# Kernel optimization log

Measured on AMD Instinct MI355X. Metric: run time of the kernel, lower is better.

Reference implementation:

```python
import jax, jax.numpy as jnp
import numpy as np

HEAD_DIM = 16

def setup_inputs() -> dict:
    key = jax.random.key(0)
    ks = jax.random.split(key, 6)
    b, m, n, e, k, d = 2, 2048, 2048, 128, 8, HEAD_DIM
    # xavier-uniform-like scale for [e, d] fan
    s = float(np.sqrt(6.0 / (e + d)))
    return {
        "x": jax.random.normal(ks[0], (b, m, e), dtype=jnp.float32),
        "y": jax.random.normal(ks[1], (b, n, e), dtype=jnp.float32),
        "lambda1": jax.random.uniform(ks[2], (k, e, d), jnp.float32, -s, s),
        "lambda2": jax.random.uniform(ks[3], (k, e, d), jnp.float32, -s, s),
        "theta1": jax.random.uniform(ks[4], (k, e, d), jnp.float32, -s, s),
        "theta2": jax.random.uniform(ks[5], (k, e, d), jnp.float32, -s, s),
        "bias_lambda": jnp.zeros((k, d), jnp.float32),
        "bias_theta": jnp.zeros((k, d), jnp.float32),
    }

def reference(x, y, lambda1, lambda2, theta1, theta2, bias_lambda, bias_theta):
    head_dim = lambda1.shape[-1]
    # r: [b, m, k, d]
    r = jnp.einsum('bmp,kpd->bmkd', x, lambda1) + bias_lambda
    # dot_att: [k, b, m, n] (bilinear QK via per-head projections of x and y)
    dot_att = jnp.einsum('bmkd,kqd,bnq->kbmn', r, lambda2, y)
    dot_att = dot_att * (head_dim ** -0.5)
    # softmax over the query/m axis (-2), NOT the key axis
    att = jax.nn.softmax(dot_att, axis=-2)
    # combine: [b, n, k, d]
    r2 = jnp.einsum('kbmn,bmp,kpd->bnkd', att, x, theta1) + bias_theta
    # output: [b, n, emb_dim_x]
    return jnp.einsum('bnkd,kqd->bnq', r2, theta2)
```

## Files before the change

kernel.cpp:

```cpp
#include <hip/hip_runtime.h>
#include <math.h>

#define BB 2
#define MM 2048
#define NN 2048
#define EE 128
#define KH 8
#define DD 16
#define NHEADS (BB * KH)
#define MSPLIT 8
#define MCHUNK (MM / MSPLIT)
#define LOG2E 1.44269504088896340736f
#define QSCALE (0.25f * LOG2E)
#define DEFER_THR 8.0f

typedef __bf16 bf16x8 __attribute__((ext_vector_type(8)));
typedef __bf16 bf16x4 __attribute__((ext_vector_type(4)));
typedef float  f32x16 __attribute__((ext_vector_type(16)));
typedef float  f32x4  __attribute__((ext_vector_type(4)));

__device__ inline bf16x8 cvt8(float4 a, float4 b) {
    bf16x8 r;
    r[0] = (__bf16)a.x; r[1] = (__bf16)a.y; r[2] = (__bf16)a.z; r[3] = (__bf16)a.w;
    r[4] = (__bf16)b.x; r[5] = (__bf16)b.y; r[6] = (__bf16)b.z; r[7] = (__bf16)b.w;
    return r;
}

__global__ __launch_bounds__(256) void proj_kernel(
    const float* __restrict__ x, const float* __restrict__ y,
    const float* __restrict__ lambda1, const float* __restrict__ lambda2,
    const float* __restrict__ theta1, const float* __restrict__ bias_lambda,
    __bf16* __restrict__ rK, __bf16* __restrict__ kyQ, __bf16* __restrict__ Vt)
{
    const int grp  = blockIdx.x;
    const int f    = blockIdx.y;
    const int head = blockIdx.z;
    const int b = head >> 3, kh = head & 7;
    const int wave = threadIdx.x >> 6;
    const int lane = threadIdx.x & 63;
    const int l15 = lane & 15, g4 = lane >> 4;

    const float* W   = ((f == 0) ? lambda1 : (f == 1) ? theta1 : lambda2)
                       + (size_t)kh * EE * DD;
    const float* src = ((f == 2) ? y : x) + (size_t)b * MM * EE;

    bf16x8 wf[4];
    #pragma unroll
    for (int kb = 0; kb < 4; ++kb) {
        const float* wp = W + (size_t)(32 * kb + 8 * g4) * DD + l15;
        bf16x8 t;
        #pragma unroll
        for (int e = 0; e < 8; ++e) t[e] = (__bf16)wp[e * DD];
        wf[kb] = t;
    }
    const float bl = (f == 0) ? bias_lambda[kh * DD + l15] : 0.f;

    for (int i = 0; i < 4; ++i) {
        const int m0 = (grp * 16 + wave * 4 + i) * 16;
        const float* xp = src + (size_t)(m0 + l15) * EE + 8 * g4;

        f32x4 acc;
        #pragma unroll
        for (int r = 0; r < 4; ++r) acc[r] = 0.f;

        #pragma unroll
        for (int kb = 0; kb < 4; ++kb) {
            float4 a = *(const float4*)(xp + 32 * kb);
            float4 c = *(const float4*)(xp + 32 * kb + 4);
            bf16x8 xf = cvt8(a, c);
            if (f == 1) acc = __builtin_amdgcn_mfma_f32_16x16x32_bf16(wf[kb], xf, acc, 0, 0, 0);
            else        acc = __builtin_amdgcn_mfma_f32_16x16x32_bf16(xf, wf[kb], acc, 0, 0, 0);
        }

        if (f == 0) {
            #pragma unroll
            for (int r = 0; r < 4; ++r)
                rK[((size_t)head * MM + m0 + 4 * g4 + r) * DD + l15] = (__bf16)(acc[r] + bl);
        } else if (f == 2) {
            #pragma unroll
            for (int r = 0; r < 4; ++r)
                kyQ[((size_t)head * NN + m0 + 4 * g4 + r) * DD + l15] = (__bf16)(acc[r] * QSCALE);
        } else {
            #pragma unroll
            for (int r = 0; r < 4; ++r)
                Vt[((size_t)head * DD + 4 * g4 + r) * MM + m0 + l15] = (__bf16)acc[r];
        }
    }
}

__global__ __launch_bounds__(256) void attn_kernel(
    const __bf16* __restrict__ rK, const __bf16* __restrict__ kyQ,
    const __bf16* __restrict__ Vt,
    float* __restrict__ Opart, float* __restrict__ mlP)
{
    __shared__ __bf16 Pst[4][32][40];

    const int tid  = threadIdx.x;
    const int wave = tid >> 6;
    const int lane = tid & 63;
    const int head = blockIdx.x >> 4;
    const int nbase = (blockIdx.x & 15) * 128 + wave * 32;
    const int ms   = blockIdx.y;
    const int b = head >> 3, kh = head & 7;

    const int l31 = lane & 31;
    const int hi  = lane >> 5;
    const int l15 = lane & 15;
    const int g4  = lane >> 4;

    const bf16x8 qf = *reinterpret_cast<const bf16x8*>(
        kyQ + ((size_t)head * NN + nbase + l31) * DD + 8 * hi);

    f32x4 o0, o1;
    #pragma unroll
    for (int i = 0; i < 4; ++i) { o0[i] = 0.f; o1[i] = 0.f; }
    float mmax = -INFINITY, lsum = 0.f;

    const __bf16* kb = rK + (size_t)head * MM * DD;
    const __bf16* vb = Vt + (size_t)head * DD * MM;

    for (int it = 0; it < MCHUNK / 32; ++it) {
        const int m0 = ms * MCHUNK + it * 32;

        const bf16x8 kf = *reinterpret_cast<const bf16x8*>(
            kb + ((size_t)(m0 + l31)) * DD + 8 * hi);

        f32x16 s;
        #pragma unroll
        for (int i = 0; i < 16; ++i) s[i] = 0.f;
        s = __builtin_amdgcn_mfma_f32_32x32x16_bf16(kf, qf, s, 0, 0, 0);

        float tm = s[0];
        #pragma unroll
        for (int r = 1; r < 16; ++r) tm = fmaxf(tm, s[r]);
        tm = fmaxf(tm, __shfl_xor(tm, 32));

        if (!__all(tm - mmax <= DEFER_THR)) {
            const float newm = fmaxf(mmax, tm);
            const float c = exp2f(mmax - newm);
            lsum *= c;
            #pragma unroll
            for (int r = 0; r < 4; ++r) {
                o0[r] *= __shfl(c, 4 * g4 + r);
                o1[r] *= __shfl(c, 16 + 4 * g4 + r);
            }
            mmax = newm;
        }

        float p[16];
        float ps = 0.f;
        #pragma unroll
        for (int r = 0; r < 16; ++r) { p[r] = exp2f(s[r] - mmax); ps += p[r]; }
        ps += __shfl_xor(ps, 32);
        lsum += ps;

        #pragma unroll
        for (int qd = 0; qd < 4; ++qd) {
            bf16x4 pk;
            pk[0] = (__bf16)p[4 * qd + 0];
            pk[1] = (__bf16)p[4 * qd + 1];
            pk[2] = (__bf16)p[4 * qd + 2];
            pk[3] = (__bf16)p[4 * qd + 3];
            *reinterpret_cast<bf16x4*>(&Pst[wave][l31][8 * qd + 4 * hi]) = pk;
        }

        const bf16x8 vf = *reinterpret_cast<const bf16x8*>(
            vb + (size_t)l15 * MM + m0 + 8 * g4);

        const bf16x8 pa0 = *reinterpret_cast<const bf16x8*>(&Pst[wave][l15][8 * g4]);
        const bf16x8 pa1 = *reinterpret_cast<const bf16x8*>(&Pst[wave][16 + l15][8 * g4]);

        o0 = __builtin_amdgcn_mfma_f32_16x16x32_bf16(pa0, vf, o0, 0, 0, 0);
        o1 = __builtin_amdgcn_mfma_f32_16x16x32_bf16(pa1, vf, o1, 0, 0, 0);
    }

    float* obase = Opart + (((size_t)ms * BB + b) * NN) * (KH * DD) + kh * DD;
    #pragma unroll
    for (int r = 0; r < 4; ++r) {
        const int n0 = nbase + 4 * g4 + r;
        const int n1 = n0 + 16;
        obase[(size_t)n0 * (KH * DD) + l15] = o0[r];
        obase[(size_t)n1 * (KH * DD) + l15] = o1[r];
    }
    if (lane < 32) {
        const size_t mlbase = (((size_t)ms * BB + b) * NN + nbase + l31) * (KH * 2) + kh * 2;
        mlP[mlbase]     = mmax;
        mlP[mlbase + 1] = lsum;
    }
}

__global__ __launch_bounds__(256) void combine_kernel(
    const float* __restrict__ Opart, const float* __restrict__ mlP,
    const float* __restrict__ bias_theta, const float* __restrict__ theta2,
    float* __restrict__ out)
{
    __shared__ float r2s[4][128];

    const int blk = blockIdx.x;
    const int b   = blk >> 9;
    const int n0  = (blk & 511) * 4;
    const int tid = threadIdx.x;

    if (tid < 128) {
        const int n_loc = tid >> 5;
        const int k  = (tid >> 2) & 7;
        const int dq = tid & 3;
        const int n = n0 + n_loc;

        float mm[MSPLIT], ls[MSPLIT];
        float Mx = -INFINITY;
        #pragma unroll
        for (int s = 0; s < MSPLIT; ++s) {
            const size_t base = (((size_t)s * BB + b) * NN + n) * (KH * 2) + k * 2;
            mm[s] = mlP[base];
            ls[s] = mlP[base + 1];
            Mx = fmaxf(Mx, mm[s]);
        }
        float L = 0.f;
        float4 O = make_float4(0.f, 0.f, 0.f, 0.f);
        #pragma unroll
        for (int s = 0; s < MSPLIT; ++s) {
            const float w = exp2f(mm[s] - Mx);
            L = fmaf(ls[s], w, L);
            const float4 op = *(const float4*)(
                Opart + (((size_t)s * BB + b) * NN + n) * (KH * DD) + k * DD + dq * 4);
            O.x = fmaf(w, op.x, O.x); O.y = fmaf(w, op.y, O.y);
            O.z = fmaf(w, op.z, O.z); O.w = fmaf(w, op.w, O.w);
        }
        const float inv = 1.f / L;
        const float* bt = bias_theta + k * DD + dq * 4;
        float4 res;
        res.x = fmaf(O.x, inv, bt[0]);
        res.y = fmaf(O.y, inv, bt[1]);
        res.z = fmaf(O.z, inv, bt[2]);
        res.w = fmaf(O.w, inv, bt[3]);
        *(float4*)&r2s[n_loc][k * DD + dq * 4] = res;
    }
    __syncthreads();
    {
        const int q   = tid & 127;
        const int nl0 = tid >> 7;
        float acc0 = 0.f, acc1 = 0.f;
        #pragma unroll
        for (int k = 0; k < KH; ++k) {
            const float4* t2 = (const float4*)(theta2 + ((size_t)k * EE + q) * DD);
            const float4* ra = (const float4*)&r2s[nl0][k * DD];
            const float4* rb = (const float4*)&r2s[nl0 + 2][k * DD];
            #pragma unroll
            for (int j = 0; j < 4; ++j) {
                const float4 t = t2[j];
                const float4 a = ra[j];
                const float4 bq = rb[j];
                acc0 = fmaf(a.x, t.x, acc0);  acc0 = fmaf(a.y, t.y, acc0);
                acc0 = fmaf(a.z, t.z, acc0);  acc0 = fmaf(a.w, t.w, acc0);
                acc1 = fmaf(bq.x, t.x, acc1); acc1 = fmaf(bq.y, t.y, acc1);
                acc1 = fmaf(bq.z, t.z, acc1); acc1 = fmaf(bq.w, t.w, acc1);
            }
        }
        out[((size_t)b * NN + n0 + nl0) * EE + q]     = acc0;
        out[((size_t)b * NN + n0 + nl0 + 2) * EE + q] = acc1;
    }
}

extern "C" void kernel_launch(void* const* d_in, const int* in_sizes, int n_in,
                              void* d_out, int out_size, void* d_ws, size_t ws_size,
                              hipStream_t stream) {
    const float* x           = (const float*)d_in[0];
    const float* y           = (const float*)d_in[1];
    const float* lambda1     = (const float*)d_in[2];
    const float* lambda2     = (const float*)d_in[3];
    const float* theta1      = (const float*)d_in[4];
    const float* theta2      = (const float*)d_in[5];
    const float* bias_lambda = (const float*)d_in[6];
    const float* bias_theta  = (const float*)d_in[7];
    float* out = (float*)d_out;

    char* w = (char*)d_ws;
    __bf16* rK  = (__bf16*)w;  w += (size_t)NHEADS * MM * DD * 2;
    __bf16* kyQ = (__bf16*)w;  w += (size_t)NHEADS * NN * DD * 2;
    __bf16* Vt  = (__bf16*)w;  w += (size_t)NHEADS * DD * MM * 2;
    float* Opart = (float*)w;  w += (size_t)MSPLIT * BB * NN * KH * DD * 4;
    float* mlP   = (float*)w;

    hipLaunchKernelGGL(proj_kernel, dim3(8, 3, 16), dim3(256), 0, stream,
                       x, y, lambda1, lambda2, theta1, bias_lambda, rK, kyQ, Vt);
    hipLaunchKernelGGL(attn_kernel, dim3(256, MSPLIT), dim3(256), 0, stream,
                       rK, kyQ, Vt, Opart, mlP);
    hipLaunchKernelGGL(combine_kernel, dim3(1024), dim3(256), 0, stream,
                       Opart, mlP, bias_theta, theta2, out);
}
```

Measured before the change: 116.3 us.

## Spread projection over more blocks, unroll attention loop, widen combine threads

The projection kernel gives each wave a single 16-row tile instead of looping over four, and its grid grows fourfold to compensate, so more blocks run in parallel. The attention loop is fully unrolled, the V load is issued before the QK MFMA, the row max uses a tree reduction, and the probabilities reuse the score registers. The m/l pair is stored and loaded as float2. The combine stage now uses all 256 threads, each handling two elements instead of four with half the block idle. This adds block-launch overhead and register pressure from unrolling in exchange for more parallelism and latency hiding.

```diff
diff --git a/kernel.cpp b/kernel.cpp
--- a/kernel.cpp
+++ b/kernel.cpp
@@ -55,36 +55,34 @@
     }
     const float bl = (f == 0) ? bias_lambda[kh * DD + l15] : 0.f;
 
-    for (int i = 0; i < 4; ++i) {
-        const int m0 = (grp * 16 + wave * 4 + i) * 16;
-        const float* xp = src + (size_t)(m0 + l15) * EE + 8 * g4;
-
-        f32x4 acc;
-        #pragma unroll
-        for (int r = 0; r < 4; ++r) acc[r] = 0.f;
-
-        #pragma unroll
-        for (int kb = 0; kb < 4; ++kb) {
-            float4 a = *(const float4*)(xp + 32 * kb);
-            float4 c = *(const float4*)(xp + 32 * kb + 4);
-            bf16x8 xf = cvt8(a, c);
-            if (f == 1) acc = __builtin_amdgcn_mfma_f32_16x16x32_bf16(wf[kb], xf, acc, 0, 0, 0);
-            else        acc = __builtin_amdgcn_mfma_f32_16x16x32_bf16(xf, wf[kb], acc, 0, 0, 0);
-        }
-
-        if (f == 0) {
-            #pragma unroll
-            for (int r = 0; r < 4; ++r)
-                rK[((size_t)head * MM + m0 + 4 * g4 + r) * DD + l15] = (__bf16)(acc[r] + bl);
-        } else if (f == 2) {
-            #pragma unroll
-            for (int r = 0; r < 4; ++r)
-                kyQ[((size_t)head * NN + m0 + 4 * g4 + r) * DD + l15] = (__bf16)(acc[r] * QSCALE);
-        } else {
-            #pragma unroll
-            for (int r = 0; r < 4; ++r)
-                Vt[((size_t)head * DD + 4 * g4 + r) * MM + m0 + l15] = (__bf16)acc[r];
-        }
+    const int m0 = (grp * 4 + wave) * 16;
+    const float* xp = src + (size_t)(m0 + l15) * EE + 8 * g4;
+
+    f32x4 acc;
+    #pragma unroll
+    for (int r = 0; r < 4; ++r) acc[r] = 0.f;
+
+    #pragma unroll
+    for (int kb = 0; kb < 4; ++kb) {
+        float4 a = *(const float4*)(xp + 32 * kb);
+        float4 c = *(const float4*)(xp + 32 * kb + 4);
+        bf16x8 xf = cvt8(a, c);
+        if (f == 1) acc = __builtin_amdgcn_mfma_f32_16x16x32_bf16(wf[kb], xf, acc, 0, 0, 0);
+        else        acc = __builtin_amdgcn_mfma_f32_16x16x32_bf16(xf, wf[kb], acc, 0, 0, 0);
+    }
+
+    if (f == 0) {
+        #pragma unroll
+        for (int r = 0; r < 4; ++r)
+            rK[((size_t)head * MM + m0 + 4 * g4 + r) * DD + l15] = (__bf16)(acc[r] + bl);
+    } else if (f == 2) {
+        #pragma unroll
+        for (int r = 0; r < 4; ++r)
+            kyQ[((size_t)head * NN + m0 + 4 * g4 + r) * DD + l15] = (__bf16)(acc[r] * QSCALE);
+    } else {
+        #pragma unroll
+        for (int r = 0; r < 4; ++r)
+            Vt[((size_t)head * DD + 4 * g4 + r) * MM + m0 + l15] = (__bf16)acc[r];
     }
 }
 
@@ -119,20 +117,26 @@
     const __bf16* kb = rK + (size_t)head * MM * DD;
     const __bf16* vb = Vt + (size_t)head * DD * MM;
 
+    #pragma unroll
     for (int it = 0; it < MCHUNK / 32; ++it) {
         const int m0 = ms * MCHUNK + it * 32;
 
         const bf16x8 kf = *reinterpret_cast<const bf16x8*>(
             kb + ((size_t)(m0 + l31)) * DD + 8 * hi);
+        const bf16x8 vf = *reinterpret_cast<const bf16x8*>(
+            vb + (size_t)l15 * MM + m0 + 8 * g4);
 
         f32x16 s;
         #pragma unroll
         for (int i = 0; i < 16; ++i) s[i] = 0.f;
         s = __builtin_amdgcn_mfma_f32_32x32x16_bf16(kf, qf, s, 0, 0, 0);
 
-        float tm = s[0];
-        #pragma unroll
-        for (int r = 1; r < 16; ++r) tm = fmaxf(tm, s[r]);
+        float t0 = fmaxf(fmaxf(s[0], s[1]), s[2]);
+        float t1 = fmaxf(fmaxf(s[3], s[4]), s[5]);
+        float t2 = fmaxf(fmaxf(s[6], s[7]), s[8]);
+        float t3 = fmaxf(fmaxf(s[9], s[10]), s[11]);
+        float t4 = fmaxf(fmaxf(s[12], s[13]), s[14]);
+        float tm = fmaxf(fmaxf(fmaxf(t0, t1), t2), fmaxf(fmaxf(t3, t4), s[15]));
         tm = fmaxf(tm, __shfl_xor(tm, 32));
 
         if (!__all(tm - mmax <= DEFER_THR)) {
@@ -147,25 +151,21 @@
             mmax = newm;
         }
 
-        float p[16];
         float ps = 0.f;
         #pragma unroll
-        for (int r = 0; r < 16; ++r) { p[r] = exp2f(s[r] - mmax); ps += p[r]; }
+        for (int r = 0; r < 16; ++r) { s[r] = exp2f(s[r] - mmax); ps += s[r]; }
         ps += __shfl_xor(ps, 32);
         lsum += ps;
 
         #pragma unroll
         for (int qd = 0; qd < 4; ++qd) {
             bf16x4 pk;
-            pk[0] = (__bf16)p[4 * qd + 0];
-            pk[1] = (__bf16)p[4 * qd + 1];
-            pk[2] = (__bf16)p[4 * qd + 2];
-            pk[3] = (__bf16)p[4 * qd + 3];
+            pk[0] = (__bf16)s[4 * qd + 0];
+            pk[1] = (__bf16)s[4 * qd + 1];
+            pk[2] = (__bf16)s[4 * qd + 2];
+            pk[3] = (__bf16)s[4 * qd + 3];
             *reinterpret_cast<bf16x4*>(&Pst[wave][l31][8 * qd + 4 * hi]) = pk;
         }
-
-        const bf16x8 vf = *reinterpret_cast<const bf16x8*>(
-            vb + (size_t)l15 * MM + m0 + 8 * g4);
 
         const bf16x8 pa0 = *reinterpret_cast<const bf16x8*>(&Pst[wave][l15][8 * g4]);
         const bf16x8 pa1 = *reinterpret_cast<const bf16x8*>(&Pst[wave][16 + l15][8 * g4]);
@@ -183,9 +183,8 @@
         obase[(size_t)n1 * (KH * DD) + l15] = o1[r];
     }
     if (lane < 32) {
-        const size_t mlbase = (((size_t)ms * BB + b) * NN + nbase + l31) * (KH * 2) + kh * 2;
-        mlP[mlbase]     = mmax;
-        mlP[mlbase + 1] = lsum;
+        float2* mlb = (float2*)(mlP + (((size_t)ms * BB + b) * NN + nbase + l31) * (KH * 2) + kh * 2);
+        *mlb = make_float2(mmax, lsum);
     }
 }
 
@@ -201,40 +200,39 @@
     const int n0  = (blk & 511) * 4;
     const int tid = threadIdx.x;
 
-    if (tid < 128) {
-        const int n_loc = tid >> 5;
-        const int k  = (tid >> 2) & 7;
-        const int dq = tid & 3;
+    {
+        const int n_loc = tid >> 6;
+        const int k  = (tid >> 3) & 7;
+        const int dh = tid & 7;
         const int n = n0 + n_loc;
 
         float mm[MSPLIT], ls[MSPLIT];
         float Mx = -INFINITY;
         #pragma unroll
         for (int s = 0; s < MSPLIT; ++s) {
-            const size_t base = (((size_t)s * BB + b) * NN + n) * (KH * 2) + k * 2;
-            mm[s] = mlP[base];
-            ls[s] = mlP[base + 1];
+            const float2 ml = *(const float2*)(
+                mlP + (((size_t)s * BB + b) * NN + n) * (KH * 2) + k * 2);
+            mm[s] = ml.x;
+            ls[s] = ml.y;
             Mx = fmaxf(Mx, mm[s]);
         }
         float L = 0.f;
-        float4 O = make_float4(0.f, 0.f, 0.f, 0.f);
+        float2 O = make_float2(0.f, 0.f);
         #pragma unroll
         for (int s = 0; s < MSPLIT; ++s) {
             const float w = exp2f(mm[s] - Mx);
             L = fmaf(ls[s], w, L);
-            const float4 op = *(const float4*)(
-                Opart + (((size_t)s * BB + b) * NN + n) * (KH * DD) + k * DD + dq * 4);
-            O.x = fmaf(w, op.x, O.x); O.y = fmaf(w, op.y, O.y);
-            O.z = fmaf(w, op.z, O.z); O.w = fmaf(w, op.w, O.w);
+            const float2 op = *(const float2*)(
+                Opart + (((size_t)s * BB + b) * NN + n) * (KH * DD) + k * DD + dh * 2);
+            O.x = fmaf(w, op.x, O.x);
+            O.y = fmaf(w, op.y, O.y);
         }
         const float inv = 1.f / L;
-        const float* bt = bias_theta + k * DD + dq * 4;
-        float4 res;
+        const float* bt = bias_theta + k * DD + dh * 2;
+        float2 res;
         res.x = fmaf(O.x, inv, bt[0]);
         res.y = fmaf(O.y, inv, bt[1]);
-        res.z = fmaf(O.z, inv, bt[2]);
-        res.w = fmaf(O.w, inv, bt[3]);
-        *(float4*)&r2s[n_loc][k * DD + dq * 4] = res;
+        *(float2*)&r2s[n_loc][k * DD + dh * 2] = res;
     }
     __syncthreads();
     {
@@ -282,7 +280,7 @@
     float* Opart = (float*)w;  w += (size_t)MSPLIT * BB * NN * KH * DD * 4;
     float* mlP   = (float*)w;
 
-    hipLaunchKernelGGL(proj_kernel, dim3(8, 3, 16), dim3(256), 0, stream,
+    hipLaunchKernelGGL(proj_kernel, dim3(32, 3, 16), dim3(256), 0, stream,
                        x, y, lambda1, lambda2, theta1, bias_lambda, rK, kyQ, Vt);
     hipLaunchKernelGGL(attn_kernel, dim3(256, MSPLIT), dim3(256), 0, stream,
                        rK, kyQ, Vt, Opart, mlP);
```

Measured after the change: 116.4 us. About the same (+0.1%).
